# Kernel optimization log

Measured on AMD Instinct MI355X. Metric: run time of the kernel, lower is better.

The kernel has to match this reference:

```python
import math
import jax, jax.numpy as jnp
import numpy as np

HEADS = 4

def setup_inputs() -> dict:
    key = jax.random.key(0)
    ks = jax.random.split(key, 6)
    B, CK, CV, T, H, W = 2, 64, 512, 8, 32, 32
    return {
        "mk": jax.random.normal(ks[0], (B, CK, T, H, W), dtype=jnp.float32),
        "qk": jax.random.normal(ks[1], (B, CK, H, W), dtype=jnp.float32),
        "ms": jax.random.uniform(ks[2], (B, T, H, W), dtype=jnp.float32),
        "qe": jax.random.uniform(ks[3], (B, CK, H, W), dtype=jnp.float32),
        "mv": jax.random.normal(ks[4], (B, CV, T, H, W), dtype=jnp.float32),
        "qv": jax.random.normal(ks[5], (B, CV, H, W), dtype=jnp.float32),
    }

def reference(mk, qk, ms, qe, mv, qv):
    B, CK, T, H, W = mk.shape
    CV = mv.shape[1]
    THW, HW = T * H * W, H * W
    c = CK // HEADS

    # head split: [B, heads, c, THW] / [B, heads, c, HW]
    mk_h = mk.reshape(B, HEADS, c, THW)
    qk_h = qk.reshape(B, HEADS, c, HW)
    qe_h = qe.reshape(B, HEADS, c, HW)

    mk_t = jnp.swapaxes(mk_h, 2, 3)  # [B, heads, THW, c]
    # qe-weighted L2-style similarity with cubic terms
    a_sq = jnp.einsum('bhnc,bhcm->bhnm', mk_t ** 3, qe_h)          # [B,h,THW,HW]
    two_ab = 2.0 * jnp.einsum('bhnc,bhcm->bhnm', mk_t, qk_h * qe_h)
    b_sq = jnp.sum(qe_h * qk_h ** 3, axis=2, keepdims=True)        # [B,h,1,HW]
    similarity = -a_sq + two_ab - b_sq                              # [B,h,THW,HW]

    # shrinkage scaling: ms -> [B,1,THW,1], broadcast over heads
    similarity = similarity * ms.reshape(B, 1, THW, 1) / math.sqrt(CK)

    # softmax over the HEAD axis (dim=1), as in the original code
    affinity = jax.nn.softmax(similarity, axis=1)                   # [B,h,THW,HW]

    # readout: per-head batched matmul over memory positions
    mo = mv.reshape(B, HEADS, CV // HEADS, THW)
    mem = jnp.einsum('bhcn,bhnm->bhcm', mo, affinity).reshape(B, CV, H, W)
    return jnp.concatenate([mem, qv], axis=1)                       # [B, 2*CV, H, W]
```

## Files before the change

kernel.cpp:

```cpp
#include <hip/hip_runtime.h>

typedef float f4 __attribute__((ext_vector_type(4)));
typedef short s4 __attribute__((ext_vector_type(4)));
typedef short s8 __attribute__((ext_vector_type(8)));

#define HWD    1024
#define THW    8192
#define CVD    512
#define MT     64
#define NC     8
#define NRANGE 1024
#define NSUB   32
#define SUBS   32
#define AFP    36

#define MFMA16 __builtin_amdgcn_mfma_f32_16x16x32_bf16

__device__ __forceinline__ unsigned short f2bf(float x) {
    unsigned u = __builtin_bit_cast(unsigned, x);
    u += 0x7fffu + ((u >> 16) & 1u);
    return (unsigned short)(u >> 16);
}
__device__ __forceinline__ float bf2f(unsigned short b) {
    unsigned u = ((unsigned)b) << 16;
    return __builtin_bit_cast(float, u);
}

__global__ __launch_bounds__(256)
void mr_init(const float* __restrict__ qv, float* __restrict__ out) {
    int idx = blockIdx.x * 256 + threadIdx.x;
    int b   = idx >> 18;
    int r   = idx & 262143;
    int ch  = r >> 8;
    float4 v = make_float4(0.f, 0.f, 0.f, 0.f);
    if (ch >= CVD) {
        v = ((const float4*)qv)[(b << 17) + ((ch - CVD) << 8) + (r & 255)];
    }
    ((float4*)out)[idx] = v;
}

__global__ __launch_bounds__(256)
void prep_mv(const float* __restrict__ mv, short* __restrict__ mvH, short* __restrict__ mvL) {
    int i = blockIdx.x * 256 + threadIdx.x;
    f4 v = ((const f4*)mv)[i];
    s4 hi, lo;
#pragma unroll
    for (int e = 0; e < 4; ++e) {
        unsigned short h = f2bf(v[e]);
        hi[e] = (short)h;
        lo[e] = (short)f2bf(v[e] - bf2f(h));
    }
    ((s4*)mvH)[i] = hi;
    ((s4*)mvL)[i] = lo;
}

__global__ __launch_bounds__(256)
void prep_feat(const float* __restrict__ mk, short* __restrict__ ftH, short* __restrict__ ftL) {
    __shared__ float mkT[16][260];
    const int bid = blockIdx.x;
    const int chunk = bid & 31, h = (bid >> 5) & 3, b = bid >> 7;
    const int t = threadIdx.x;
    const float* src = mk + (size_t)(b * 64 + h * 16) * THW + chunk * 256;
#pragma unroll
    for (int i = 0; i < 4; ++i) {
        int q = t + 256 * i;
        int c = q >> 6, j = q & 63;
        *(f4*)&mkT[c][j * 4] = *(const f4*)(src + (size_t)c * THW + j * 4);
    }
    __syncthreads();
    unsigned uH[16], uL[16];
#pragma unroll
    for (int c = 0; c < 16; ++c) {
        float x  = mkT[c][t];
        float x3 = x * x * x;
        unsigned short h3 = f2bf(x3), h1 = f2bf(x);
        unsigned short l3 = f2bf(x3 - bf2f(h3)), l1 = f2bf(x - bf2f(h1));
        uH[c] = (unsigned)h3 | ((unsigned)h1 << 16);
        uL[c] = (unsigned)l3 | ((unsigned)l1 << 16);
    }
    size_t row = ((size_t)(b * 4 + h) * THW + chunk * 256 + t) * 32;
    uint4* dH = (uint4*)(ftH + row);
    uint4* dL = (uint4*)(ftL + row);
#pragma unroll
    for (int k = 0; k < 4; ++k) {
        dH[k] = make_uint4(uH[4*k], uH[4*k+1], uH[4*k+2], uH[4*k+3]);
        dL[k] = make_uint4(uL[4*k], uL[4*k+1], uL[4*k+2], uL[4*k+3]);
    }
}

__global__ __launch_bounds__(512, 4)
void mr_main(const float* __restrict__ qk, const float* __restrict__ qe,
             const float* __restrict__ ms,
             const short* __restrict__ mvH, const short* __restrict__ mvL,
             const short* __restrict__ ftH, const short* __restrict__ ftL,
             float* __restrict__ out)
{
    __shared__ short wSH[4][MT][AFP];
    __shared__ short wSL[4][MT][AFP];
    __shared__ short affS[2][2][MT][AFP];
    __shared__ float msS[NRANGE];
    __shared__ float bS[4][MT];

    const int bid  = blockIdx.x;
    const int wid  = (bid & 7) * 64 + (bid >> 3);
    const int nc   = wid >> 6;
    const int rest = wid & 63;
    const int mt0  = rest & 15;
    const int hp   = (rest >> 4) & 1;
    const int b    = rest >> 5;
    const int m0   = mt0 * MT;
    const int n0   = nc * NRANGE;

    const int t  = threadIdx.x;
    const int wv = t >> 6, l = t & 63, lr = l & 15, lg = l >> 4;
    const int nt = wv & 1, mq = wv >> 1;
    const int hl = wv & 1, cvh = (wv >> 1) & 1, mh = (wv >> 2) & 1;

    if (t < 256) {
        ((f4*)msS)[t] = ((const f4*)(ms + (size_t)b * THW + n0))[t];
        const int h = t >> 6, m = t & 63;
        const float* qkp = qk + (size_t)(b * 64 + h * 16) * HWD + m0 + m;
        const float* qep = qe + (size_t)(b * 64 + h * 16) * HWD + m0 + m;
        float bias = 0.f;
#pragma unroll
        for (int c = 0; c < 16; ++c) {
            float kv = qkp[(size_t)c * HWD];
            float ev = qep[(size_t)c * HWD];
            float w0 = -ev, w1 = 2.f * kv * ev;
            unsigned short h0 = f2bf(w0), h1w = f2bf(w1);
            unsigned short l0 = f2bf(w0 - bf2f(h0)), l1 = f2bf(w1 - bf2f(h1w));
            *(unsigned*)&wSH[h][m][2 * c] = (unsigned)h0 | ((unsigned)h1w << 16);
            *(unsigned*)&wSL[h][m][2 * c] = (unsigned)l0 | ((unsigned)l1 << 16);
            bias -= ev * kv * kv * kv;
        }
        bS[h][m] = bias;
    }
    __syncthreads();

    float biasr[4];
#pragma unroll
    for (int h = 0; h < 4; ++h) biasr[h] = bS[h][mq * 16 + lr];

    f4 acc[4][2];
#pragma unroll
    for (int ct = 0; ct < 4; ++ct) {
        acc[ct][0] = f4{0.f, 0.f, 0.f, 0.f};
        acc[ct][1] = f4{0.f, 0.f, 0.f, 0.f};
    }

    for (int s = 0; s < SUBS; ++s) {
        const int ns = s * NSUB;

        f4 sacc[4];
        {
            const int nrow = n0 + ns + nt * 16 + lr;
#pragma unroll
            for (int h = 0; h < 4; ++h) {
                size_t fo = ((size_t)(b * 4 + h) * THW + nrow) * 32 + lg * 8;
                s8 fH = *(const s8*)(ftH + fo);
                s8 fL = *(const s8*)(ftL + fo);
                const short* wrH = &wSH[h][mq * 16 + lr][lg * 8];
                const short* wrL = &wSL[h][mq * 16 + lr][lg * 8];
                s8 wH = __builtin_shufflevector(*(const s4*)wrH, *(const s4*)(wrH + 4), 0,1,2,3,4,5,6,7);
                s8 wL = __builtin_shufflevector(*(const s4*)wrL, *(const s4*)(wrL + 4), 0,1,2,3,4,5,6,7);
                f4 sa = f4{0.f, 0.f, 0.f, 0.f};
                sa = MFMA16(fH, wH, sa, 0, 0, 0);
                sa = MFMA16(fL, wH, sa, 0, 0, 0);
                sa = MFMA16(fH, wL, sa, 0, 0, 0);
                sacc[h] = sa;
            }
        }
        s8 aHr[4], aLr[4];
#pragma unroll
        for (int ct = 0; ct < 4; ++ct) {
            size_t ao = ((size_t)(b * CVD + hp * 256 + hl * 128 + cvh * 64 + ct * 16 + lr)) * THW
                        + n0 + ns + lg * 8;
            aHr[ct] = *(const s8*)(mvH + ao);
            aLr[ct] = *(const s8*)(mvL + ao);
        }
        {
            f4 msv = *(const f4*)&msS[ns + nt * 16 + lg * 4];
            short hi0[4], hi1[4], lo0[4], lo1[4];
#pragma unroll
            for (int r = 0; r < 4; ++r) {
                float x[4];
#pragma unroll
                for (int h = 0; h < 4; ++h)
                    x[h] = (sacc[h][r] + biasr[h]) * msv[r] * 0.125f;
                float mx = fmaxf(fmaxf(x[0], x[1]), fmaxf(x[2], x[3]));
                float e0 = __expf(x[0] - mx), e1 = __expf(x[1] - mx);
                float e2 = __expf(x[2] - mx), e3 = __expf(x[3] - mx);
                float rin = 1.f / (e0 + e1 + e2 + e3);
                float a0 = (hp ? e2 : e0) * rin;
                float a1 = (hp ? e3 : e1) * rin;
                unsigned short hA = f2bf(a0), hB = f2bf(a1);
                hi0[r] = (short)hA; lo0[r] = (short)f2bf(a0 - bf2f(hA));
                hi1[r] = (short)hB; lo1[r] = (short)f2bf(a1 - bf2f(hB));
            }
            const int mrow = mq * 16 + lr, nn = nt * 16 + lg * 4;
            *(s4*)&affS[0][0][mrow][nn] = s4{hi0[0], hi0[1], hi0[2], hi0[3]};
            *(s4*)&affS[1][0][mrow][nn] = s4{lo0[0], lo0[1], lo0[2], lo0[3]};
            *(s4*)&affS[0][1][mrow][nn] = s4{hi1[0], hi1[1], hi1[2], hi1[3]};
            *(s4*)&affS[1][1][mrow][nn] = s4{lo1[0], lo1[1], lo1[2], lo1[3]};
        }
        __syncthreads();

        {
            s8 bH[2], bL[2];
#pragma unroll
            for (int mt = 0; mt < 2; ++mt) {
                const short* pH = &affS[0][hl][mh * 32 + mt * 16 + lr][lg * 8];
                const short* pL = &affS[1][hl][mh * 32 + mt * 16 + lr][lg * 8];
                bH[mt] = __builtin_shufflevector(*(const s4*)pH, *(const s4*)(pH + 4), 0,1,2,3,4,5,6,7);
                bL[mt] = __builtin_shufflevector(*(const s4*)pL, *(const s4*)(pL + 4), 0,1,2,3,4,5,6,7);
            }
#pragma unroll
            for (int ct = 0; ct < 4; ++ct)
#pragma unroll
                for (int mt = 0; mt < 2; ++mt) {
                    acc[ct][mt] = MFMA16(aHr[ct], bH[mt], acc[ct][mt], 0, 0, 0);
                    acc[ct][mt] = MFMA16(aLr[ct], bH[mt], acc[ct][mt], 0, 0, 0);
                    acc[ct][mt] = MFMA16(aHr[ct], bL[mt], acc[ct][mt], 0, 0, 0);
                }
        }
        __syncthreads();
    }

    float* ob = out + (size_t)b * (2 * CVD * HWD);
#pragma unroll
    for (int ct = 0; ct < 4; ++ct)
#pragma unroll
        for (int mt = 0; mt < 2; ++mt)
#pragma unroll
            for (int r = 0; r < 4; ++r) {
                const int cv = hp * 256 + hl * 128 + cvh * 64 + ct * 16 + lg * 4 + r;
                const int m  = m0 + mh * 32 + mt * 16 + lr;
#if defined(__HIP_PLATFORM_AMD__)
                unsafeAtomicAdd(ob + (size_t)cv * HWD + m, acc[ct][mt][r]);
#else
                atomicAdd(ob + (size_t)cv * HWD + m, acc[ct][mt][r]);
#endif
            }
}

extern "C" void kernel_launch(void* const* d_in, const int* in_sizes, int n_in,
                              void* d_out, int out_size, void* d_ws, size_t ws_size,
                              hipStream_t stream) {
    (void)in_sizes; (void)n_in; (void)out_size; (void)ws_size;
    const float* mk = (const float*)d_in[0];
    const float* qk = (const float*)d_in[1];
    const float* ms = (const float*)d_in[2];
    const float* qe = (const float*)d_in[3];
    const float* mv = (const float*)d_in[4];
    const float* qv = (const float*)d_in[5];
    float* out = (float*)d_out;

    short* mvH = (short*)d_ws;
    short* mvL = (short*)((char*)d_ws + 16777216);
    short* ftH = (short*)((char*)d_ws + 33554432);
    short* ftL = (short*)((char*)d_ws + 37748736);

    mr_init<<<2048, 256, 0, stream>>>(qv, out);
    prep_mv<<<8192, 256, 0, stream>>>(mv, mvH, mvL);
    prep_feat<<<256, 256, 0, stream>>>(mk, ftH, ftL);
    mr_main<<<512, 512, 0, stream>>>(qk, qe, ms, mvH, mvL, ftH, ftL, out);
}
```

Baseline: 288.8 us.

## Merge prep kernels, halve main-kernel tile, use packed bf16 conversion

The three preprocessing kernels become one launch that dispatches on block index. Rounding now uses the hardware packed v_cvt_pk_bf16_f32 instruction instead of manual bit arithmetic. The main kernel uses 32-row query tiles with 256 threads and 1024 blocks, which removes redundant similarity work across the former mh halves and raises parallelism. It also keeps the high weight fragment in registers, folds the bias into the MFMA accumulator init, and overlays shared memory with a union. The trade-off is more blocks, each reloading its feature and value tiles, plus more atomic traffic.

```diff
diff --git a/kernel.cpp b/kernel.cpp
--- a/kernel.cpp
+++ b/kernel.cpp
@@ -7,118 +7,116 @@
 #define HWD    1024
 #define THW    8192
 #define CVD    512
-#define MT     64
-#define NC     8
+#define MT     32
 #define NRANGE 1024
-#define NSUB   32
 #define SUBS   32
 #define AFP    36
 
 #define MFMA16 __builtin_amdgcn_mfma_f32_16x16x32_bf16
 
-__device__ __forceinline__ unsigned short f2bf(float x) {
-    unsigned u = __builtin_bit_cast(unsigned, x);
-    u += 0x7fffu + ((u >> 16) & 1u);
-    return (unsigned short)(u >> 16);
-}
-__device__ __forceinline__ float bf2f(unsigned short b) {
-    unsigned u = ((unsigned)b) << 16;
+__device__ __forceinline__ unsigned cvtpk(float a, float b) {
+    unsigned r;
+    asm volatile("v_cvt_pk_bf16_f32 %0, %1, %2" : "=v"(r) : "v"(a), "v"(b));
+    return r;
+}
+__device__ __forceinline__ float ubits(unsigned u) {
     return __builtin_bit_cast(float, u);
 }
+__device__ __forceinline__ s8 frag2(const short* p) {
+    return __builtin_shufflevector(*(const s4*)p, *(const s4*)(p + 4), 0,1,2,3,4,5,6,7);
+}
 
 __global__ __launch_bounds__(256)
-void mr_init(const float* __restrict__ qv, float* __restrict__ out) {
-    int idx = blockIdx.x * 256 + threadIdx.x;
-    int b   = idx >> 18;
-    int r   = idx & 262143;
-    int ch  = r >> 8;
-    float4 v = make_float4(0.f, 0.f, 0.f, 0.f);
-    if (ch >= CVD) {
-        v = ((const float4*)qv)[(b << 17) + ((ch - CVD) << 8) + (r & 255)];
-    }
-    ((float4*)out)[idx] = v;
-}
-
-__global__ __launch_bounds__(256)
-void prep_mv(const float* __restrict__ mv, short* __restrict__ mvH, short* __restrict__ mvL) {
-    int i = blockIdx.x * 256 + threadIdx.x;
-    f4 v = ((const f4*)mv)[i];
-    s4 hi, lo;
-#pragma unroll
-    for (int e = 0; e < 4; ++e) {
-        unsigned short h = f2bf(v[e]);
-        hi[e] = (short)h;
-        lo[e] = (short)f2bf(v[e] - bf2f(h));
-    }
-    ((s4*)mvH)[i] = hi;
-    ((s4*)mvL)[i] = lo;
-}
-
-__global__ __launch_bounds__(256)
-void prep_feat(const float* __restrict__ mk, short* __restrict__ ftH, short* __restrict__ ftL) {
+void mr_prep(const float* __restrict__ mv, const float* __restrict__ qv,
+             const float* __restrict__ mk,
+             short* __restrict__ mvH, short* __restrict__ mvL,
+             short* __restrict__ ftH, short* __restrict__ ftL,
+             float* __restrict__ out)
+{
     __shared__ float mkT[16][260];
-    const int bid = blockIdx.x;
-    const int chunk = bid & 31, h = (bid >> 5) & 3, b = bid >> 7;
-    const int t = threadIdx.x;
-    const float* src = mk + (size_t)(b * 64 + h * 16) * THW + chunk * 256;
-#pragma unroll
-    for (int i = 0; i < 4; ++i) {
-        int q = t + 256 * i;
-        int c = q >> 6, j = q & 63;
-        *(f4*)&mkT[c][j * 4] = *(const f4*)(src + (size_t)c * THW + j * 4);
-    }
-    __syncthreads();
-    unsigned uH[16], uL[16];
-#pragma unroll
-    for (int c = 0; c < 16; ++c) {
-        float x  = mkT[c][t];
-        float x3 = x * x * x;
-        unsigned short h3 = f2bf(x3), h1 = f2bf(x);
-        unsigned short l3 = f2bf(x3 - bf2f(h3)), l1 = f2bf(x - bf2f(h1));
-        uH[c] = (unsigned)h3 | ((unsigned)h1 << 16);
-        uL[c] = (unsigned)l3 | ((unsigned)l1 << 16);
-    }
-    size_t row = ((size_t)(b * 4 + h) * THW + chunk * 256 + t) * 32;
-    uint4* dH = (uint4*)(ftH + row);
-    uint4* dL = (uint4*)(ftL + row);
-#pragma unroll
-    for (int k = 0; k < 4; ++k) {
-        dH[k] = make_uint4(uH[4*k], uH[4*k+1], uH[4*k+2], uH[4*k+3]);
-        dL[k] = make_uint4(uL[4*k], uL[4*k+1], uL[4*k+2], uL[4*k+3]);
-    }
-}
-
-__global__ __launch_bounds__(512, 4)
+    const int bid = blockIdx.x, t = threadIdx.x;
+    if (bid < 8192) {
+        int i = bid * 256 + t;
+        f4 v = ((const f4*)mv)[i];
+        unsigned h01 = cvtpk(v[0], v[1]);
+        unsigned h23 = cvtpk(v[2], v[3]);
+        float f0 = ubits(h01 << 16), f1 = ubits(h01 & 0xffff0000u);
+        float f2 = ubits(h23 << 16), f3 = ubits(h23 & 0xffff0000u);
+        unsigned l01 = cvtpk(v[0] - f0, v[1] - f1);
+        unsigned l23 = cvtpk(v[2] - f2, v[3] - f3);
+        ((uint2*)mvH)[i] = make_uint2(h01, h23);
+        ((uint2*)mvL)[i] = make_uint2(l01, l23);
+    } else if (bid < 10240) {
+        int idx = (bid - 8192) * 256 + t;
+        int b = idx >> 18, r = idx & 262143, ch = r >> 8;
+        f4 v = f4{0.f, 0.f, 0.f, 0.f};
+        if (ch >= CVD) v = ((const f4*)qv)[(b << 17) + ((ch - CVD) << 8) + (r & 255)];
+        ((f4*)out)[idx] = v;
+    } else {
+        const int fbid = bid - 10240;
+        const int chunk = fbid & 31, h = (fbid >> 5) & 3, b = fbid >> 7;
+        const float* src = mk + (size_t)(b * 64 + h * 16) * THW + chunk * 256;
+#pragma unroll
+        for (int i = 0; i < 4; ++i) {
+            int q = t + 256 * i;
+            int c = q >> 6, j = q & 63;
+            *(f4*)&mkT[c][j * 4] = *(const f4*)(src + (size_t)c * THW + j * 4);
+        }
+        __syncthreads();
+        unsigned uH[16], uL[16];
+#pragma unroll
+        for (int c = 0; c < 16; ++c) {
+            float x = mkT[c][t];
+            float x3 = x * x * x;
+            unsigned hh = cvtpk(x3, x);
+            float r3 = x3 - ubits(hh << 16);
+            float r1 = x  - ubits(hh & 0xffff0000u);
+            uH[c] = hh;
+            uL[c] = cvtpk(r3, r1);
+        }
+        size_t row = ((size_t)(b * 4 + h) * THW + chunk * 256 + t) * 32;
+        uint4* dH = (uint4*)(ftH + row);
+        uint4* dL = (uint4*)(ftL + row);
+#pragma unroll
+        for (int k = 0; k < 4; ++k) {
+            dH[k] = make_uint4(uH[4*k], uH[4*k+1], uH[4*k+2], uH[4*k+3]);
+            dL[k] = make_uint4(uL[4*k], uL[4*k+1], uL[4*k+2], uL[4*k+3]);
+        }
+    }
+}
+
+__global__ __launch_bounds__(256, 4)
 void mr_main(const float* __restrict__ qk, const float* __restrict__ qe,
              const float* __restrict__ ms,
              const short* __restrict__ mvH, const short* __restrict__ mvL,
              const short* __restrict__ ftH, const short* __restrict__ ftL,
              float* __restrict__ out)
 {
-    __shared__ short wSH[4][MT][AFP];
-    __shared__ short wSL[4][MT][AFP];
-    __shared__ short affS[2][2][MT][AFP];
-    __shared__ float msS[NRANGE];
+    union SM {
+        struct { short wH[4][MT][AFP]; } su;
+        struct { short aff[2][2][MT][AFP]; float msv[NRANGE]; } mn;
+    };
+    __shared__ __align__(16) SM sm;
+    __shared__ __align__(16) short wLs[4][MT][AFP];
     __shared__ float bS[4][MT];
 
     const int bid  = blockIdx.x;
-    const int wid  = (bid & 7) * 64 + (bid >> 3);
-    const int nc   = wid >> 6;
-    const int rest = wid & 63;
-    const int mt0  = rest & 15;
-    const int hp   = (rest >> 4) & 1;
-    const int b    = rest >> 5;
+    const int wid  = (bid & 7) * 128 + (bid >> 3);
+    const int nc   = wid >> 7;
+    const int rest = wid & 127;
+    const int mt0  = rest & 31;
+    const int hp   = (rest >> 5) & 1;
+    const int b    = rest >> 6;
     const int m0   = mt0 * MT;
     const int n0   = nc * NRANGE;
 
     const int t  = threadIdx.x;
     const int wv = t >> 6, l = t & 63, lr = l & 15, lg = l >> 4;
     const int nt = wv & 1, mq = wv >> 1;
-    const int hl = wv & 1, cvh = (wv >> 1) & 1, mh = (wv >> 2) & 1;
-
-    if (t < 256) {
-        ((f4*)msS)[t] = ((const f4*)(ms + (size_t)b * THW + n0))[t];
-        const int h = t >> 6, m = t & 63;
+    const int hl = wv & 1, cvh = wv >> 1;
+
+    if (t < 128) {
+        const int h = t >> 5, m = t & 31;
         const float* qkp = qk + (size_t)(b * 64 + h * 16) * HWD + m0 + m;
         const float* qep = qe + (size_t)(b * 64 + h * 16) * HWD + m0 + m;
         float bias = 0.f;
@@ -127,19 +125,26 @@
             float kv = qkp[(size_t)c * HWD];
             float ev = qep[(size_t)c * HWD];
             float w0 = -ev, w1 = 2.f * kv * ev;
-            unsigned short h0 = f2bf(w0), h1w = f2bf(w1);
-            unsigned short l0 = f2bf(w0 - bf2f(h0)), l1 = f2bf(w1 - bf2f(h1w));
-            *(unsigned*)&wSH[h][m][2 * c] = (unsigned)h0 | ((unsigned)h1w << 16);
-            *(unsigned*)&wSL[h][m][2 * c] = (unsigned)l0 | ((unsigned)l1 << 16);
+            unsigned hh = cvtpk(w0, w1);
+            float r0 = w0 - ubits(hh << 16);
+            float r1 = w1 - ubits(hh & 0xffff0000u);
+            *(unsigned*)&sm.su.wH[h][m][2 * c] = hh;
+            *(unsigned*)&wLs[h][m][2 * c]      = cvtpk(r0, r1);
             bias -= ev * kv * kv * kv;
         }
         bS[h][m] = bias;
     }
     __syncthreads();
 
+    s8 wHr[4];
     float biasr[4];
 #pragma unroll
-    for (int h = 0; h < 4; ++h) biasr[h] = bS[h][mq * 16 + lr];
+    for (int h = 0; h < 4; ++h) {
+        wHr[h]   = frag2(&sm.su.wH[h][mq * 16 + lr][lg * 8]);
+        biasr[h] = bS[h][mq * 16 + lr];
+    }
+    ((f4*)sm.mn.msv)[t] = ((const f4*)(ms + (size_t)b * THW + n0))[t];
+    __syncthreads();
 
     f4 acc[4][2];
 #pragma unroll
@@ -148,81 +153,79 @@
         acc[ct][1] = f4{0.f, 0.f, 0.f, 0.f};
     }
 
+    const size_t fstep  = (size_t)THW * 32;
+    const short* fbaseH = ftH + ((size_t)(b * 4) * THW + n0 + nt * 16 + lr) * 32 + lg * 8;
+    const short* fbaseL = ftL + ((size_t)(b * 4) * THW + n0 + nt * 16 + lr) * 32 + lg * 8;
+    const size_t abase0 = ((size_t)(b * CVD + hp * 256 + hl * 128 + cvh * 64 + lr)) * THW
+                          + n0 + lg * 8;
+
     for (int s = 0; s < SUBS; ++s) {
-        const int ns = s * NSUB;
+        const int ns = s * 32;
 
         f4 sacc[4];
-        {
-            const int nrow = n0 + ns + nt * 16 + lr;
-#pragma unroll
-            for (int h = 0; h < 4; ++h) {
-                size_t fo = ((size_t)(b * 4 + h) * THW + nrow) * 32 + lg * 8;
-                s8 fH = *(const s8*)(ftH + fo);
-                s8 fL = *(const s8*)(ftL + fo);
-                const short* wrH = &wSH[h][mq * 16 + lr][lg * 8];
-                const short* wrL = &wSL[h][mq * 16 + lr][lg * 8];
-                s8 wH = __builtin_shufflevector(*(const s4*)wrH, *(const s4*)(wrH + 4), 0,1,2,3,4,5,6,7);
-                s8 wL = __builtin_shufflevector(*(const s4*)wrL, *(const s4*)(wrL + 4), 0,1,2,3,4,5,6,7);
-                f4 sa = f4{0.f, 0.f, 0.f, 0.f};
-                sa = MFMA16(fH, wH, sa, 0, 0, 0);
-                sa = MFMA16(fL, wH, sa, 0, 0, 0);
-                sa = MFMA16(fH, wL, sa, 0, 0, 0);
-                sacc[h] = sa;
-            }
-        }
+#pragma unroll
+        for (int h = 0; h < 4; ++h) {
+            s8 fH = *(const s8*)(fbaseH + (size_t)h * fstep + (size_t)ns * 32);
+            s8 fL = *(const s8*)(fbaseL + (size_t)h * fstep + (size_t)ns * 32);
+            s8 wL = frag2(&wLs[h][mq * 16 + lr][lg * 8]);
+            f4 sa = f4{biasr[h], biasr[h], biasr[h], biasr[h]};
+            sa = MFMA16(fH, wHr[h], sa, 0, 0, 0);
+            sa = MFMA16(fL, wHr[h], sa, 0, 0, 0);
+            sa = MFMA16(fH, wL,     sa, 0, 0, 0);
+            sacc[h] = sa;
+        }
+
         s8 aHr[4], aLr[4];
 #pragma unroll
         for (int ct = 0; ct < 4; ++ct) {
-            size_t ao = ((size_t)(b * CVD + hp * 256 + hl * 128 + cvh * 64 + ct * 16 + lr)) * THW
-                        + n0 + ns + lg * 8;
+            size_t ao = abase0 + (size_t)ct * 16 * THW + ns;
             aHr[ct] = *(const s8*)(mvH + ao);
             aLr[ct] = *(const s8*)(mvL + ao);
         }
+
+        f4 msv4 = *(const f4*)&sm.mn.msv[ns + nt * 16 + lg * 4];
+        float a0[4], a1[4];
+#pragma unroll
+        for (int r = 0; r < 4; ++r) {
+            const float sc = msv4[r] * 0.125f;
+            float x0 = sacc[0][r] * sc, x1 = sacc[1][r] * sc;
+            float x2 = sacc[2][r] * sc, x3 = sacc[3][r] * sc;
+            float mx = fmaxf(fmaxf(x0, x1), fmaxf(x2, x3));
+            float e0 = __expf(x0 - mx), e1 = __expf(x1 - mx);
+            float e2 = __expf(x2 - mx), e3 = __expf(x3 - mx);
+            float rin = 1.f / (e0 + e1 + e2 + e3);
+            a0[r] = (hp ? e2 : e0) * rin;
+            a1[r] = (hp ? e3 : e1) * rin;
+        }
+        unsigned h001 = cvtpk(a0[0], a0[1]), h023 = cvtpk(a0[2], a0[3]);
+        unsigned h101 = cvtpk(a1[0], a1[1]), h123 = cvtpk(a1[2], a1[3]);
+        unsigned l001 = cvtpk(a0[0] - ubits(h001 << 16), a0[1] - ubits(h001 & 0xffff0000u));
+        unsigned l023 = cvtpk(a0[2] - ubits(h023 << 16), a0[3] - ubits(h023 & 0xffff0000u));
+        unsigned l101 = cvtpk(a1[0] - ubits(h101 << 16), a1[1] - ubits(h101 & 0xffff0000u));
+        unsigned l123 = cvtpk(a1[2] - ubits(h123 << 16), a1[3] - ubits(h123 & 0xffff0000u));
         {
-            f4 msv = *(const f4*)&msS[ns + nt * 16 + lg * 4];
-            short hi0[4], hi1[4], lo0[4], lo1[4];
-#pragma unroll
-            for (int r = 0; r < 4; ++r) {
-                float x[4];
-#pragma unroll
-                for (int h = 0; h < 4; ++h)
-                    x[h] = (sacc[h][r] + biasr[h]) * msv[r] * 0.125f;
-                float mx = fmaxf(fmaxf(x[0], x[1]), fmaxf(x[2], x[3]));
-                float e0 = __expf(x[0] - mx), e1 = __expf(x[1] - mx);
-                float e2 = __expf(x[2] - mx), e3 = __expf(x[3] - mx);
-                float rin = 1.f / (e0 + e1 + e2 + e3);
-                float a0 = (hp ? e2 : e0) * rin;
-                float a1 = (hp ? e3 : e1) * rin;
-                unsigned short hA = f2bf(a0), hB = f2bf(a1);
-                hi0[r] = (short)hA; lo0[r] = (short)f2bf(a0 - bf2f(hA));
-                hi1[r] = (short)hB; lo1[r] = (short)f2bf(a1 - bf2f(hB));
+            const int mrow = mq * 16 + lr, nn = nt * 16 + lg * 4;
+            *(uint2*)&sm.mn.aff[0][0][mrow][nn] = make_uint2(h001, h023);
+            *(uint2*)&sm.mn.aff[1][0][mrow][nn] = make_uint2(l001, l023);
+            *(uint2*)&sm.mn.aff[0][1][mrow][nn] = make_uint2(h101, h123);
+            *(uint2*)&sm.mn.aff[1][1][mrow][nn] = make_uint2(l101, l123);
+        }
+        __syncthreads();
+
+        s8 bH[2], bL[2];
+#pragma unroll
+        for (int mt = 0; mt < 2; ++mt) {
+            bH[mt] = frag2(&sm.mn.aff[0][hl][mt * 16 + lr][lg * 8]);
+            bL[mt] = frag2(&sm.mn.aff[1][hl][mt * 16 + lr][lg * 8]);
+        }
+#pragma unroll
+        for (int ct = 0; ct < 4; ++ct)
+#pragma unroll
+            for (int mt = 0; mt < 2; ++mt) {
+                acc[ct][mt] = MFMA16(aHr[ct], bH[mt], acc[ct][mt], 0, 0, 0);
+                acc[ct][mt] = MFMA16(aLr[ct], bH[mt], acc[ct][mt], 0, 0, 0);
+                acc[ct][mt] = MFMA16(aHr[ct], bL[mt], acc[ct][mt], 0, 0, 0);
             }
-            const int mrow = mq * 16 + lr, nn = nt * 16 + lg * 4;
-            *(s4*)&affS[0][0][mrow][nn] = s4{hi0[0], hi0[1], hi0[2], hi0[3]};
-            *(s4*)&affS[1][0][mrow][nn] = s4{lo0[0], lo0[1], lo0[2], lo0[3]};
-            *(s4*)&affS[0][1][mrow][nn] = s4{hi1[0], hi1[1], hi1[2], hi1[3]};
-            *(s4*)&affS[1][1][mrow][nn] = s4{lo1[0], lo1[1], lo1[2], lo1[3]};
-        }
-        __syncthreads();
-
-        {
-            s8 bH[2], bL[2];
-#pragma unroll
-            for (int mt = 0; mt < 2; ++mt) {
-                const short* pH = &affS[0][hl][mh * 32 + mt * 16 + lr][lg * 8];
-                const short* pL = &affS[1][hl][mh * 32 + mt * 16 + lr][lg * 8];
-                bH[mt] = __builtin_shufflevector(*(const s4*)pH, *(const s4*)(pH + 4), 0,1,2,3,4,5,6,7);
-                bL[mt] = __builtin_shufflevector(*(const s4*)pL, *(const s4*)(pL + 4), 0,1,2,3,4,5,6,7);
-            }
-#pragma unroll
-            for (int ct = 0; ct < 4; ++ct)
-#pragma unroll
-                for (int mt = 0; mt < 2; ++mt) {
-                    acc[ct][mt] = MFMA16(aHr[ct], bH[mt], acc[ct][mt], 0, 0, 0);
-                    acc[ct][mt] = MFMA16(aLr[ct], bH[mt], acc[ct][mt], 0, 0, 0);
-                    acc[ct][mt] = MFMA16(aHr[ct], bL[mt], acc[ct][mt], 0, 0, 0);
-                }
-        }
         __syncthreads();
     }
 
@@ -234,7 +237,7 @@
 #pragma unroll
             for (int r = 0; r < 4; ++r) {
                 const int cv = hp * 256 + hl * 128 + cvh * 64 + ct * 16 + lg * 4 + r;
-                const int m  = m0 + mh * 32 + mt * 16 + lr;
+                const int m  = m0 + mt * 16 + lr;
 #if defined(__HIP_PLATFORM_AMD__)
                 unsafeAtomicAdd(ob + (size_t)cv * HWD + m, acc[ct][mt][r]);
 #else
@@ -260,8 +263,6 @@
     short* ftH = (short*)((char*)d_ws + 33554432);
     short* ftL = (short*)((char*)d_ws + 37748736);
 
-    mr_init<<<2048, 256, 0, stream>>>(qv, out);
-    prep_mv<<<8192, 256, 0, stream>>>(mv, mvH, mvL);
-    prep_feat<<<256, 256, 0, stream>>>(mk, ftH, ftL);
-    mr_main<<<512, 512, 0, stream>>>(qk, qe, ms, mvH, mvL, ftH, ftL, out);
-}
+    mr_prep<<<10496, 256, 0, stream>>>(mv, qv, mk, mvH, mvL, ftH, ftL, out);
+    mr_main<<<1024, 256, 0, stream>>>(qk, qe, ms, mvH, mvL, ftH, ftL, out);
+}
```

After: 302.9 us. 4.9% more time.
